# Kernel optimization log

Measured on AMD Instinct MI355X. Metric: run time of the kernel, lower is better.

## Reference

```python
import jax, jax.numpy as jnp
import numpy as np

B, C, H, W = 4, 256, 64, 64
D, K = 256, 32
EPS = 1e-12  # F.normalize clamp

def setup_inputs() -> dict:
    key = jax.random.key(0)
    k1, k2, k3, k4 = jax.random.split(key, 4)
    x = jax.random.normal(k1, (B, C, H, W), dtype=jnp.float32)
    w_theta = jax.random.normal(k2, (D, C), dtype=jnp.float32) * 0.05  # 1x1 conv theta
    w_phi = jax.random.normal(k3, (K, C // K), dtype=jnp.float32) * 0.1  # grouped 1x1 conv phi
    scale = jax.random.uniform(k4, (D, K), dtype=jnp.float32, minval=-1.0, maxval=0.0)
    return {"x": x, "w_theta": w_theta, "w_phi": w_phi, "scale": scale}

def reference(x, w_theta, w_phi, scale):
    b, c, h, w = x.shape
    d, k = scale.shape
    n = h * w
    xf = x.reshape(b, c, n)                                   # B,D,N (C==D)
    # --- Gen_code ---
    xg = xf.reshape(b, k, c // k, n)                          # grouped 1x1 conv
    x_phi = jnp.einsum('bkcn,kc->bnk', xg, w_phi)             # B,N,K
    x_phi = jax.nn.softmax(x_phi, axis=1)                     # softmax over pixels
    x_theta = jnp.einsum('dc,bcn->bdn', w_theta, xf)          # B,D,N
    code = jnp.einsum('bdn,bnk->bdk', x_theta, x_phi)         # B,D,K
    code = code / jnp.maximum(jnp.linalg.norm(code, axis=1, keepdims=True), EPS)
    # (dropout p=0.15 treated as identity)
    # --- embedded residual, without materializing B,N,D,K ---
    s2 = scale * scale                                        # D,K
    t1 = jnp.einsum('bdn,dk->bnk', xf * xf, s2)
    t2 = jnp.einsum('bdn,bdk->bnk', xf, s2[None] * code)
    t3 = jnp.einsum('dk,bdk->bk', s2, code * code)
    dist = t1 - 2.0 * t2 + t3[:, None, :]                     # sum_d (scale*(x-code))^2
    Q = jax.nn.softmax(-0.5 * dist, axis=2)                   # B,N,K
    Qsum = Q.sum(axis=1)                                      # B,K
    # Z_[b,d,k] = sum_n Q*residual / Qsum = scale*(sum_n Q x / Qsum - code)
    Z_ = scale[None] * (jnp.einsum('bdn,bnk->bdk', xf, Q) / Qsum[:, None, :] - code)
    Z = Z_ / jnp.sqrt((Z_ * Z_).sum(axis=1, keepdims=True))   # torch sqrt, no eps
    return Z, Q
```

## Files before the change

kernel.cpp:

```cpp
#include <hip/hip_runtime.h>
#include <math.h>

#define BB 4
#define CC 256
#define NN 4096
#define KK 32
#define DD 256
#define GG 8
#define NT2 64
#define NE 8

__device__ __forceinline__ float wredsum(float v) {
#pragma unroll
  for (int o = 32; o > 0; o >>= 1) v += __shfl_xor(v, o, 64);
  return v;
}

__global__ __launch_bounds__(256) void k_phi(const float* __restrict__ x,
                                             const float* __restrict__ wphi,
                                             float* __restrict__ phi,
                                             float* __restrict__ Sp) {
  const int half = blockIdx.x & 1;
  const int k = (blockIdx.x >> 1) & 31;
  const int b = blockIdx.x >> 6;
  const int tid = threadIdx.x;
  const float* xb = x + (size_t)(b * CC + k * GG) * NN + half * 2048;
  float w[GG];
#pragma unroll
  for (int j = 0; j < GG; ++j) w[j] = wphi[k * GG + j];
  float4 v[2];
  float sum = 0.f;
#pragma unroll
  for (int i = 0; i < 2; ++i) {
    const int n = i * 1024 + tid * 4;
    float4 s = make_float4(0.f, 0.f, 0.f, 0.f);
#pragma unroll
    for (int j = 0; j < GG; ++j) {
      const float4 xv = *reinterpret_cast<const float4*>(xb + (size_t)j * NN + n);
      s.x = fmaf(xv.x, w[j], s.x);
      s.y = fmaf(xv.y, w[j], s.y);
      s.z = fmaf(xv.z, w[j], s.z);
      s.w = fmaf(xv.w, w[j], s.w);
    }
    v[i].x = __expf(s.x);
    v[i].y = __expf(s.y);
    v[i].z = __expf(s.z);
    v[i].w = __expf(s.w);
    sum += v[i].x + v[i].y + v[i].z + v[i].w;
  }
  float* pk = phi + (size_t)(b * KK + k) * NN + half * 2048;
#pragma unroll
  for (int i = 0; i < 2; ++i) {
    *reinterpret_cast<float4*>(pk + i * 1024 + tid * 4) = v[i];
  }
  __shared__ float rb[4];
  sum = wredsum(sum);
  if ((tid & 63) == 0) rb[tid >> 6] = sum;
  __syncthreads();
  if (tid == 0)
    Sp[((size_t)half * BB + b) * KK + k] = rb[0] + rb[1] + rb[2] + rb[3];
}

__global__ __launch_bounds__(256) void k_xpT(const float* __restrict__ x,
                                             const float* __restrict__ phi,
                                             float* __restrict__ m1e) {
  const int e = blockIdx.x & 7;
  const int ct = (blockIdx.x >> 3) & 31;
  const int b = blockIdx.x >> 8;
  const int tid = threadIdx.x;
  __shared__ float smem[256 * 33];
  const int kl = tid >> 3;
  const int nq = tid & 7;
  const int k = tid & 31;
  const int g = tid >> 5;
  const float* xb = x + (size_t)(b * CC + ct * 8) * NN + e * 512;
  float acc[8] = {0.f, 0.f, 0.f, 0.f, 0.f, 0.f, 0.f, 0.f};
#pragma unroll
  for (int ch = 0; ch < 2; ++ch) {
    const float* pch = phi + (size_t)(b * KK + kl) * NN + e * 512 + ch * 256;
#pragma unroll
    for (int j = 0; j < 8; ++j) {
      const int nn = (j * 8 + nq) * 4;
      const float4 pv = *reinterpret_cast<const float4*>(pch + nn);
      smem[(nn + 0) * 33 + kl] = pv.x;
      smem[(nn + 1) * 33 + kl] = pv.y;
      smem[(nn + 2) * 33 + kl] = pv.z;
      smem[(nn + 3) * 33 + kl] = pv.w;
    }
    __syncthreads();
#pragma unroll
    for (int i = 0; i < 8; ++i) {
      const int nl = g * 32 + i * 4;
      const float p0 = smem[(nl + 0) * 33 + k];
      const float p1 = smem[(nl + 1) * 33 + k];
      const float p2 = smem[(nl + 2) * 33 + k];
      const float p3 = smem[(nl + 3) * 33 + k];
#pragma unroll
      for (int c = 0; c < 8; ++c) {
        const float4 xv =
            *reinterpret_cast<const float4*>(xb + (size_t)c * NN + ch * 256 + nl);
        acc[c] = fmaf(xv.x, p0, acc[c]);
        acc[c] = fmaf(xv.y, p1, acc[c]);
        acc[c] = fmaf(xv.z, p2, acc[c]);
        acc[c] = fmaf(xv.w, p3, acc[c]);
      }
    }
    __syncthreads();
  }
#pragma unroll
  for (int c = 0; c < 8; ++c) smem[(g * 8 + c) * 33 + k] = acc[c];
  __syncthreads();
  const int c2 = tid & 7, k2 = tid >> 3;
  float s = 0.f;
#pragma unroll
  for (int gg = 0; gg < 8; ++gg) s += smem[(gg * 8 + c2) * 33 + k2];
  m1e[((size_t)(e * BB + b) * KK + k2) * CC + ct * 8 + c2] = s;
}

__global__ __launch_bounds__(256) void k_code(const float* __restrict__ m1e,
                                              const float* __restrict__ Sp,
                                              const float* __restrict__ wth,
                                              const float* __restrict__ scale,
                                              float* __restrict__ code,
                                              float* __restrict__ bc2,
                                              float* __restrict__ s2g,
                                              float* __restrict__ t3) {
  const int b = blockIdx.x >> 5;
  const int k = blockIdx.x & 31;
  const int d = threadIdx.x;
  const float invS =
      1.f / (Sp[(size_t)b * KK + k] + Sp[((size_t)BB + b) * KK + k]);
  __shared__ __align__(16) float m1s[CC];
  float m = 0.f;
#pragma unroll
  for (int e = 0; e < NE; ++e)
    m += m1e[((size_t)(e * BB + b) * KK + k) * CC + d];
  m1s[d] = m * invS;
  __syncthreads();
  float cd = 0.f;
  const float* wt = wth + (size_t)d * CC;
#pragma unroll 4
  for (int c = 0; c < CC; c += 4) {
    const float4 w4 = *reinterpret_cast<const float4*>(wt + c);
    const float4 m4 = *reinterpret_cast<const float4*>(&m1s[c]);
    cd = fmaf(w4.x, m4.x, cd);
    cd = fmaf(w4.y, m4.y, cd);
    cd = fmaf(w4.z, m4.z, cd);
    cd = fmaf(w4.w, m4.w, cd);
  }
  __shared__ float rb[4];
  float ss = wredsum(cd * cd);
  if ((d & 63) == 0) rb[d >> 6] = ss;
  __syncthreads();
  const float nrm = sqrtf(rb[0] + rb[1] + rb[2] + rb[3]);
  const float inv = 1.f / fmaxf(nrm, 1e-12f);
  cd *= inv;
  const float sc = scale[(size_t)d * KK + k];
  const float s2 = sc * sc;
  code[((size_t)b * DD + d) * KK + k] = cd;
  bc2[((size_t)b * DD + d) * KK + k] = 2.f * s2 * cd;
  if (b == 0) s2g[(size_t)d * KK + k] = s2;
  float tt = wredsum(s2 * cd * cd);
  __syncthreads();
  if ((d & 63) == 0) rb[d >> 6] = tt;
  __syncthreads();
  if (d == 0) t3[b * KK + k] = rb[0] + rb[1] + rb[2] + rb[3];
}

__global__ __launch_bounds__(512) void k_dist(const float* __restrict__ x,
                                              const float* __restrict__ s2g,
                                              const float* __restrict__ bc2,
                                              const float* __restrict__ t3,
                                              float* __restrict__ qout,
                                              float* __restrict__ qpart) {
  const int b = blockIdx.x >> 6;
  const int tile = blockIdx.x & 63;
  const int n0 = tile * 64;
  const int tid = threadIdx.x;
  const int lane = tid & 63;
  const int wid = __builtin_amdgcn_readfirstlane(tid >> 6);
  const int d0 = wid * 32;
  __shared__ float lds[4 * 64 * 33];
  __shared__ float smax[64 * 9];
  __shared__ float ssum[64 * 9];
  float accA[32], accB[32];
#pragma unroll
  for (int k = 0; k < 32; ++k) { accA[k] = 0.f; accB[k] = 0.f; }
  const float* xb = x + ((size_t)b * CC + d0) * NN + n0 + lane;
  const float* s2b = s2g + (size_t)d0 * KK;
  const float* bcb = bc2 + ((size_t)b * DD + d0) * KK;
#pragma unroll 2
  for (int dd = 0; dd < 32; ++dd) {
    const float xv = xb[(size_t)dd * NN];
    const float x2 = xv * xv;
    const float* s2r = s2b + dd * KK;
    const float* bcr = bcb + dd * KK;
#pragma unroll
    for (int k = 0; k < 32; ++k) {
      accA[k] = fmaf(x2, s2r[k], accA[k]);
      accB[k] = fmaf(xv, bcr[k], accB[k]);
    }
  }
  if (wid >= 4) {
    float* Lp = lds + ((size_t)((wid - 4) * 64 + lane)) * 33;
#pragma unroll
    for (int k = 0; k < 32; ++k) Lp[k] = accA[k] - accB[k];
  }
  __syncthreads();
  if (wid < 4) {
    float* Lp = lds + ((size_t)(wid * 64 + lane)) * 33;
#pragma unroll
    for (int k = 0; k < 32; ++k) Lp[k] += accA[k] - accB[k];
  }
  __syncthreads();
  const int n = lane;
  const int kq = wid;
  float vals[4];
#pragma unroll
  for (int j = 0; j < 4; ++j) {
    const int k = kq * 4 + j;
    float s = 0.f;
#pragma unroll
    for (int g = 0; g < 4; ++g) s += lds[((size_t)(g * 64 + n)) * 33 + k];
    vals[j] = -0.5f * (s + t3[b * KK + k]);
  }
  float m4 = fmaxf(fmaxf(vals[0], vals[1]), fmaxf(vals[2], vals[3]));
  smax[n * 9 + kq] = m4;
  __syncthreads();
  float m = smax[n * 9 + 0];
#pragma unroll
  for (int g = 1; g < 8; ++g) m = fmaxf(m, smax[n * 9 + g]);
  float e[4];
  float ps = 0.f;
#pragma unroll
  for (int j = 0; j < 4; ++j) {
    e[j] = __expf(vals[j] - m);
    ps += e[j];
  }
  ssum[n * 9 + kq] = ps;
  __syncthreads();
  float tot = 0.f;
#pragma unroll
  for (int g = 0; g < 8; ++g) tot += ssum[n * 9 + g];
  const float inv = 1.f / tot;
  float4 q4;
  q4.x = e[0] * inv; q4.y = e[1] * inv; q4.z = e[2] * inv; q4.w = e[3] * inv;
  *reinterpret_cast<float4*>(qout + ((size_t)b * NN + n0 + n) * KK + kq * 4) = q4;
  float qs[4] = {q4.x, q4.y, q4.z, q4.w};
#pragma unroll
  for (int j = 0; j < 4; ++j) {
    const float v = wredsum(qs[j]);
    if (n == 0) qpart[((size_t)b * KK + kq * 4 + j) * NT2 + tile] = v;
  }
}

__global__ __launch_bounds__(256) void k_xq(const float* __restrict__ x,
                                            const float* __restrict__ q,
                                            float* __restrict__ znq8) {
  const int e = blockIdx.x & 7;
  const int ct = (blockIdx.x >> 3) & 31;
  const int b = blockIdx.x >> 8;
  const int tid = threadIdx.x;
  const int k = tid & 31;
  const int g = tid >> 5;
  const int n0 = e * 512 + g * 64;
  const float* xb = x + (size_t)(b * CC + ct * 8) * NN;
  const float* qb = q + (size_t)b * NN * KK + k;
  float acc[8] = {0.f, 0.f, 0.f, 0.f, 0.f, 0.f, 0.f, 0.f};
  for (int n = n0; n < n0 + 64; n += 4) {
    const float p0 = qb[(size_t)(n + 0) * KK];
    const float p1 = qb[(size_t)(n + 1) * KK];
    const float p2 = qb[(size_t)(n + 2) * KK];
    const float p3 = qb[(size_t)(n + 3) * KK];
#pragma unroll
    for (int c = 0; c < 8; ++c) {
      const float4 xv = *reinterpret_cast<const float4*>(xb + (size_t)c * NN + n);
      acc[c] = fmaf(xv.x, p0, acc[c]);
      acc[c] = fmaf(xv.y, p1, acc[c]);
      acc[c] = fmaf(xv.z, p2, acc[c]);
      acc[c] = fmaf(xv.w, p3, acc[c]);
    }
  }
  __shared__ float lds[8 * 8 * 33];
#pragma unroll
  for (int c = 0; c < 8; ++c) lds[(g * 8 + c) * 33 + k] = acc[c];
  __syncthreads();
  const int c2 = tid & 7, k2 = tid >> 3;
  float s = 0.f;
#pragma unroll
  for (int gg = 0; gg < 8; ++gg) s += lds[(gg * 8 + c2) * 33 + k2];
  znq8[((size_t)(e * BB + b) * KK + k2) * CC + ct * 8 + c2] = s;
}

__global__ __launch_bounds__(256) void k_z(const float* __restrict__ znq8,
                                           const float* __restrict__ code,
                                           const float* __restrict__ scale,
                                           const float* __restrict__ qpart,
                                           float* __restrict__ zout) {
  const int b = blockIdx.x >> 5;
  const int k = blockIdx.x & 31;
  const int d = threadIdx.x;
  __shared__ float rb[4];
  float qp = 0.f;
  if (d < NT2) qp = qpart[((size_t)b * KK + k) * NT2 + d];
  qp = wredsum(qp);
  if ((d & 63) == 0) rb[d >> 6] = qp;
  __syncthreads();
  const float qs = rb[0] + rb[1] + rb[2] + rb[3];
  float zn = 0.f;
#pragma unroll
  for (int e = 0; e < NE; ++e)
    zn += znq8[((size_t)(e * BB + b) * KK + k) * CC + d];
  const float cd = code[((size_t)b * DD + d) * KK + k];
  const float z_ = scale[(size_t)d * KK + k] * (zn / qs - cd);
  float ss = wredsum(z_ * z_);
  __syncthreads();
  if ((d & 63) == 0) rb[d >> 6] = ss;
  __syncthreads();
  const float rn = 1.f / sqrtf(rb[0] + rb[1] + rb[2] + rb[3]);
  zout[((size_t)b * DD + d) * KK + k] = z_ * rn;
}

extern "C" void kernel_launch(void* const* d_in, const int* in_sizes, int n_in,
                              void* d_out, int out_size, void* d_ws, size_t ws_size,
                              hipStream_t stream) {
  const float* x = (const float*)d_in[0];
  const float* wth = (const float*)d_in[1];
  const float* wphi = (const float*)d_in[2];
  const float* scale = (const float*)d_in[3];
  float* out = (float*)d_out;
  float* zout = out;
  float* qout = out + (size_t)BB * DD * KK;
  float* ws = (float*)d_ws;
  float* phi = ws;
  float* Sp = phi + (size_t)BB * NN * KK;
  float* m1e = Sp + 2 * (size_t)BB * KK;
  float* code = m1e + (size_t)NE * BB * KK * CC;
  float* bc2 = code + (size_t)BB * DD * KK;
  float* s2g = bc2 + (size_t)BB * DD * KK;
  float* t3 = s2g + (size_t)DD * KK;
  float* qpart = t3 + BB * KK;
  float* znq8 = qpart + (size_t)BB * KK * NT2;

  k_phi<<<BB * KK * 2, 256, 0, stream>>>(x, wphi, phi, Sp);
  k_xpT<<<BB * 32 * NE, 256, 0, stream>>>(x, phi, m1e);
  k_code<<<BB * KK, 256, 0, stream>>>(m1e, Sp, wth, scale, code, bc2, s2g, t3);
  k_dist<<<BB * NT2, 512, 0, stream>>>(x, s2g, bc2, t3, qout, qpart);
  k_xq<<<BB * 32 * NE, 256, 0, stream>>>(x, qout, znq8);
  k_z<<<BB * KK, 256, 0, stream>>>(znq8, code, scale, qpart, zout);
}
```

Measured before the change: 78.03 us.

## Fuse epilogue kernels into producers via last-blocks atomic-counter handoff

Merges k_code into k_xpT and k_z into k_xq, cutting the launch count from six to four. Each block increments a global counter after writing its partials. The last 128 blocks to arrive spin until every block has finished, then run the per-(b,k) epilogue. This removes two launches and their gaps, but the handoff costs a spin-wait, and the counters are reset inside k_phi.

```diff
diff --git a/kernel.cpp b/kernel.cpp
--- a/kernel.cpp
+++ b/kernel.cpp
@@ -9,6 +9,8 @@
 #define GG 8
 #define NT2 64
 #define NE 8
+#define XPT_BLOCKS (BB * 32 * NE)
+#define EPI (BB * KK)
 
 __device__ __forceinline__ float wredsum(float v) {
 #pragma unroll
@@ -19,11 +21,16 @@
 __global__ __launch_bounds__(256) void k_phi(const float* __restrict__ x,
                                              const float* __restrict__ wphi,
                                              float* __restrict__ phi,
-                                             float* __restrict__ Sp) {
+                                             float* __restrict__ Sp,
+                                             int* __restrict__ cnts) {
+  const int tid = threadIdx.x;
+  if (blockIdx.x == 0 && tid == 0) {
+    __hip_atomic_store(&cnts[0], 0, __ATOMIC_RELAXED, __HIP_MEMORY_SCOPE_AGENT);
+    __hip_atomic_store(&cnts[1], 0, __ATOMIC_RELAXED, __HIP_MEMORY_SCOPE_AGENT);
+  }
   const int half = blockIdx.x & 1;
   const int k = (blockIdx.x >> 1) & 31;
   const int b = blockIdx.x >> 6;
-  const int tid = threadIdx.x;
   const float* xb = x + (size_t)(b * CC + k * GG) * NN + half * 2048;
   float w[GG];
 #pragma unroll
@@ -61,9 +68,12 @@
     Sp[((size_t)half * BB + b) * KK + k] = rb[0] + rb[1] + rb[2] + rb[3];
 }
 
-__global__ __launch_bounds__(256) void k_xpT(const float* __restrict__ x,
-                                             const float* __restrict__ phi,
-                                             float* __restrict__ m1e) {
+__global__ __launch_bounds__(256) void k_xpT_code(
+    const float* __restrict__ x, const float* __restrict__ phi,
+    float* __restrict__ m1e, const float* __restrict__ Sp,
+    const float* __restrict__ wth, const float* __restrict__ scale,
+    float* __restrict__ code, float* __restrict__ bc2,
+    float* __restrict__ s2g, float* __restrict__ t3, int* __restrict__ cnt) {
   const int e = blockIdx.x & 7;
   const int ct = (blockIdx.x >> 3) & 31;
   const int b = blockIdx.x >> 8;
@@ -110,61 +120,69 @@
 #pragma unroll
   for (int c = 0; c < 8; ++c) smem[(g * 8 + c) * 33 + k] = acc[c];
   __syncthreads();
-  const int c2 = tid & 7, k2 = tid >> 3;
-  float s = 0.f;
-#pragma unroll
-  for (int gg = 0; gg < 8; ++gg) s += smem[(gg * 8 + c2) * 33 + k2];
-  m1e[((size_t)(e * BB + b) * KK + k2) * CC + ct * 8 + c2] = s;
-}
-
-__global__ __launch_bounds__(256) void k_code(const float* __restrict__ m1e,
-                                              const float* __restrict__ Sp,
-                                              const float* __restrict__ wth,
-                                              const float* __restrict__ scale,
-                                              float* __restrict__ code,
-                                              float* __restrict__ bc2,
-                                              float* __restrict__ s2g,
-                                              float* __restrict__ t3) {
-  const int b = blockIdx.x >> 5;
-  const int k = blockIdx.x & 31;
-  const int d = threadIdx.x;
-  const float invS =
-      1.f / (Sp[(size_t)b * KK + k] + Sp[((size_t)BB + b) * KK + k]);
-  __shared__ __align__(16) float m1s[CC];
-  float m = 0.f;
-#pragma unroll
-  for (int e = 0; e < NE; ++e)
-    m += m1e[((size_t)(e * BB + b) * KK + k) * CC + d];
-  m1s[d] = m * invS;
-  __syncthreads();
-  float cd = 0.f;
-  const float* wt = wth + (size_t)d * CC;
+  {
+    const int c2 = tid & 7, k2 = tid >> 3;
+    float s = 0.f;
+#pragma unroll
+    for (int gg = 0; gg < 8; ++gg) s += smem[(gg * 8 + c2) * 33 + k2];
+    m1e[((size_t)(e * BB + b) * KK + k2) * CC + ct * 8 + c2] = s;
+  }
+  __shared__ int srank;
+  __syncthreads();
+  if (tid == 0)
+    srank = __hip_atomic_fetch_add(cnt, 1, __ATOMIC_ACQ_REL,
+                                   __HIP_MEMORY_SCOPE_AGENT);
+  __syncthreads();
+  if (srank < XPT_BLOCKS - EPI) return;
+  const int uid = srank - (XPT_BLOCKS - EPI);
+  const int bb = uid >> 5;
+  const int kk = uid & 31;
+  if (tid == 0) {
+    while (__hip_atomic_load(cnt, __ATOMIC_ACQUIRE,
+                             __HIP_MEMORY_SCOPE_AGENT) < XPT_BLOCKS)
+      __builtin_amdgcn_s_sleep(4);
+  }
+  __syncthreads();
+  (void)__hip_atomic_load(cnt, __ATOMIC_ACQUIRE, __HIP_MEMORY_SCOPE_AGENT);
+  {
+    const int d = tid;
+    float* m1s = smem;
+    __shared__ float rbx[4];
+    const float invS =
+        1.f / (Sp[(size_t)bb * KK + kk] + Sp[((size_t)BB + bb) * KK + kk]);
+    float m = 0.f;
+#pragma unroll
+    for (int e2 = 0; e2 < NE; ++e2)
+      m += m1e[(((size_t)e2 * BB + bb) * KK + kk) * CC + d];
+    m1s[d] = m * invS;
+    __syncthreads();
+    float cd = 0.f;
+    const float* wt = wth + (size_t)d * CC;
 #pragma unroll 4
-  for (int c = 0; c < CC; c += 4) {
-    const float4 w4 = *reinterpret_cast<const float4*>(wt + c);
-    const float4 m4 = *reinterpret_cast<const float4*>(&m1s[c]);
-    cd = fmaf(w4.x, m4.x, cd);
-    cd = fmaf(w4.y, m4.y, cd);
-    cd = fmaf(w4.z, m4.z, cd);
-    cd = fmaf(w4.w, m4.w, cd);
-  }
-  __shared__ float rb[4];
-  float ss = wredsum(cd * cd);
-  if ((d & 63) == 0) rb[d >> 6] = ss;
-  __syncthreads();
-  const float nrm = sqrtf(rb[0] + rb[1] + rb[2] + rb[3]);
-  const float inv = 1.f / fmaxf(nrm, 1e-12f);
-  cd *= inv;
-  const float sc = scale[(size_t)d * KK + k];
-  const float s2 = sc * sc;
-  code[((size_t)b * DD + d) * KK + k] = cd;
-  bc2[((size_t)b * DD + d) * KK + k] = 2.f * s2 * cd;
-  if (b == 0) s2g[(size_t)d * KK + k] = s2;
-  float tt = wredsum(s2 * cd * cd);
-  __syncthreads();
-  if ((d & 63) == 0) rb[d >> 6] = tt;
-  __syncthreads();
-  if (d == 0) t3[b * KK + k] = rb[0] + rb[1] + rb[2] + rb[3];
+    for (int c = 0; c < CC; c += 4) {
+      const float4 w4 = *reinterpret_cast<const float4*>(wt + c);
+      cd = fmaf(w4.x, m1s[c + 0], cd);
+      cd = fmaf(w4.y, m1s[c + 1], cd);
+      cd = fmaf(w4.z, m1s[c + 2], cd);
+      cd = fmaf(w4.w, m1s[c + 3], cd);
+    }
+    float ss = wredsum(cd * cd);
+    if ((d & 63) == 0) rbx[d >> 6] = ss;
+    __syncthreads();
+    const float nrm = sqrtf(rbx[0] + rbx[1] + rbx[2] + rbx[3]);
+    const float inv = 1.f / fmaxf(nrm, 1e-12f);
+    cd *= inv;
+    const float sc = scale[(size_t)d * KK + kk];
+    const float s2 = sc * sc;
+    code[((size_t)bb * DD + d) * KK + kk] = cd;
+    bc2[((size_t)bb * DD + d) * KK + kk] = 2.f * s2 * cd;
+    if (bb == 0) s2g[(size_t)d * KK + kk] = s2;
+    float tt = wredsum(s2 * cd * cd);
+    __syncthreads();
+    if ((d & 63) == 0) rbx[d >> 6] = tt;
+    __syncthreads();
+    if (d == 0) t3[bb * KK + kk] = rbx[0] + rbx[1] + rbx[2] + rbx[3];
+  }
 }
 
 __global__ __launch_bounds__(512) void k_dist(const float* __restrict__ x,
@@ -244,8 +262,10 @@
   for (int g = 0; g < 8; ++g) tot += ssum[n * 9 + g];
   const float inv = 1.f / tot;
   float4 q4;
-  q4.x = e[0] * inv; q4.y = e[1] * inv; q4.z = e[2] * inv; q4.w = e[3] * inv;
-  *reinterpret_cast<float4*>(qout + ((size_t)b * NN + n0 + n) * KK + kq * 4) = q4;
+  q4.x = e[0] * inv; q4.y = e[1] * inv;
+  q4.z = e[2] * inv; q4.w = e[3] * inv;
+  *reinterpret_cast<float4*>(qout + ((size_t)b * NN + n0 + n) * KK + kq * 4) =
+      q4;
   float qs[4] = {q4.x, q4.y, q4.z, q4.w};
 #pragma unroll
   for (int j = 0; j < 4; ++j) {
@@ -254,9 +274,11 @@
   }
 }
 
-__global__ __launch_bounds__(256) void k_xq(const float* __restrict__ x,
-                                            const float* __restrict__ q,
-                                            float* __restrict__ znq8) {
+__global__ __launch_bounds__(256) void k_xq_z(
+    const float* __restrict__ x, const float* __restrict__ q,
+    float* __restrict__ znq8, const float* __restrict__ code,
+    const float* __restrict__ scale, const float* __restrict__ qpart,
+    float* __restrict__ zout, int* __restrict__ cnt) {
   const int e = blockIdx.x & 7;
   const int ct = (blockIdx.x >> 3) & 31;
   const int b = blockIdx.x >> 8;
@@ -285,45 +307,56 @@
 #pragma unroll
   for (int c = 0; c < 8; ++c) lds[(g * 8 + c) * 33 + k] = acc[c];
   __syncthreads();
-  const int c2 = tid & 7, k2 = tid >> 3;
-  float s = 0.f;
-#pragma unroll
-  for (int gg = 0; gg < 8; ++gg) s += lds[(gg * 8 + c2) * 33 + k2];
-  znq8[((size_t)(e * BB + b) * KK + k2) * CC + ct * 8 + c2] = s;
-}
-
-__global__ __launch_bounds__(256) void k_z(const float* __restrict__ znq8,
-                                           const float* __restrict__ code,
-                                           const float* __restrict__ scale,
-                                           const float* __restrict__ qpart,
-                                           float* __restrict__ zout) {
-  const int b = blockIdx.x >> 5;
-  const int k = blockIdx.x & 31;
-  const int d = threadIdx.x;
-  __shared__ float rb[4];
-  float qp = 0.f;
-  if (d < NT2) qp = qpart[((size_t)b * KK + k) * NT2 + d];
-  qp = wredsum(qp);
-  if ((d & 63) == 0) rb[d >> 6] = qp;
-  __syncthreads();
-  const float qs = rb[0] + rb[1] + rb[2] + rb[3];
-  float zn = 0.f;
-#pragma unroll
-  for (int e = 0; e < NE; ++e)
-    zn += znq8[((size_t)(e * BB + b) * KK + k) * CC + d];
-  const float cd = code[((size_t)b * DD + d) * KK + k];
-  const float z_ = scale[(size_t)d * KK + k] * (zn / qs - cd);
-  float ss = wredsum(z_ * z_);
-  __syncthreads();
-  if ((d & 63) == 0) rb[d >> 6] = ss;
-  __syncthreads();
-  const float rn = 1.f / sqrtf(rb[0] + rb[1] + rb[2] + rb[3]);
-  zout[((size_t)b * DD + d) * KK + k] = z_ * rn;
+  {
+    const int c2 = tid & 7, k2 = tid >> 3;
+    float s = 0.f;
+#pragma unroll
+    for (int gg = 0; gg < 8; ++gg) s += lds[(gg * 8 + c2) * 33 + k2];
+    znq8[((size_t)(e * BB + b) * KK + k2) * CC + ct * 8 + c2] = s;
+  }
+  __shared__ int srank;
+  __syncthreads();
+  if (tid == 0)
+    srank = __hip_atomic_fetch_add(cnt, 1, __ATOMIC_ACQ_REL,
+                                   __HIP_MEMORY_SCOPE_AGENT);
+  __syncthreads();
+  if (srank < XPT_BLOCKS - EPI) return;
+  const int uid = srank - (XPT_BLOCKS - EPI);
+  const int bb = uid >> 5;
+  const int kk = uid & 31;
+  if (tid == 0) {
+    while (__hip_atomic_load(cnt, __ATOMIC_ACQUIRE,
+                             __HIP_MEMORY_SCOPE_AGENT) < XPT_BLOCKS)
+      __builtin_amdgcn_s_sleep(4);
+  }
+  __syncthreads();
+  (void)__hip_atomic_load(cnt, __ATOMIC_ACQUIRE, __HIP_MEMORY_SCOPE_AGENT);
+  {
+    const int d = tid;
+    __shared__ float rbx[4];
+    float qp = (d < NT2) ? qpart[((size_t)bb * KK + kk) * NT2 + d] : 0.f;
+    qp = wredsum(qp);
+    if ((d & 63) == 0) rbx[d >> 6] = qp;
+    __syncthreads();
+    const float qs2 = rbx[0] + rbx[1] + rbx[2] + rbx[3];
+    float zn = 0.f;
+#pragma unroll
+    for (int e2 = 0; e2 < NE; ++e2)
+      zn += znq8[(((size_t)e2 * BB + bb) * KK + kk) * CC + d];
+    const float cdv = code[((size_t)bb * DD + d) * KK + kk];
+    const float z_ = scale[(size_t)d * KK + kk] * (zn / qs2 - cdv);
+    float ss = wredsum(z_ * z_);
+    __syncthreads();
+    if ((d & 63) == 0) rbx[d >> 6] = ss;
+    __syncthreads();
+    const float rn = 1.f / sqrtf(rbx[0] + rbx[1] + rbx[2] + rbx[3]);
+    zout[((size_t)bb * DD + d) * KK + kk] = z_ * rn;
+  }
 }
 
 extern "C" void kernel_launch(void* const* d_in, const int* in_sizes, int n_in,
-                              void* d_out, int out_size, void* d_ws, size_t ws_size,
-                              hipStream_t stream) {
+                              void* d_out, int out_size, void* d_ws,
+                              size_t ws_size, hipStream_t stream) {
   const float* x = (const float*)d_in[0];
   const float* wth = (const float*)d_in[1];
   const float* wphi = (const float*)d_in[2];
@@ -341,11 +374,12 @@
   float* t3 = s2g + (size_t)DD * KK;
   float* qpart = t3 + BB * KK;
   float* znq8 = qpart + (size_t)BB * KK * NT2;
-
-  k_phi<<<BB * KK * 2, 256, 0, stream>>>(x, wphi, phi, Sp);
-  k_xpT<<<BB * 32 * NE, 256, 0, stream>>>(x, phi, m1e);
-  k_code<<<BB * KK, 256, 0, stream>>>(m1e, Sp, wth, scale, code, bc2, s2g, t3);
+  int* cnts = (int*)(znq8 + (size_t)NE * BB * KK * CC);
+
+  k_phi<<<BB * KK * 2, 256, 0, stream>>>(x, wphi, phi, Sp, cnts);
+  k_xpT_code<<<XPT_BLOCKS, 256, 0, stream>>>(x, phi, m1e, Sp, wth, scale, code,
+                                             bc2, s2g, t3, cnts);
   k_dist<<<BB * NT2, 512, 0, stream>>>(x, s2g, bc2, t3, qout, qpart);
-  k_xq<<<BB * 32 * NE, 256, 0, stream>>>(x, qout, znq8);
-  k_z<<<BB * KK, 256, 0, stream>>>(znq8, code, scale, qpart, zout);
-}
+  k_xq_z<<<XPT_BLOCKS, 256, 0, stream>>>(x, qout, znq8, code, scale, qpart,
+                                         zout, cnts + 1);
+}
```

Result: slower. 146.1 us (+87.3%).

## Store phi pixel-major and reuse one x-times-weights kernel for phi and Q

Applied to the files above, without the earlier changes.

k_phi now tiles over 64-pixel slices and computes all 32 groups per block. It transposes the exp values through LDS so phi is stored in the same [B,N,K] layout as Q, and it writes one partial sum per slice that k_code reduces. This lets the old k_xpT, with its LDS transpose and barriers, be replaced by the same simple k_xp kernel already used for x·Q. k_code also splits its dot-product accumulator into four chains for more instruction-level parallelism. The trade-off is strided 32-float loads of phi in k_xp instead of an LDS-staged transpose, and more partial sums to reduce.

```diff
diff --git a/kernel.cpp b/kernel.cpp
--- a/kernel.cpp
+++ b/kernel.cpp
@@ -9,6 +9,7 @@
 #define GG 8
 #define NT2 64
 #define NE 8
+#define NSL 64
 
 __device__ __forceinline__ float wredsum(float v) {
 #pragma unroll
@@ -19,106 +20,115 @@
 __global__ __launch_bounds__(256) void k_phi(const float* __restrict__ x,
                                              const float* __restrict__ wphi,
                                              float* __restrict__ phi,
-                                             float* __restrict__ Sp) {
-  const int half = blockIdx.x & 1;
-  const int k = (blockIdx.x >> 1) & 31;
+                                             float* __restrict__ SpE) {
   const int b = blockIdx.x >> 6;
+  const int sl = blockIdx.x & 63;
+  const int n0 = sl * 64;
   const int tid = threadIdx.x;
-  const float* xb = x + (size_t)(b * CC + k * GG) * NN + half * 2048;
-  float w[GG];
-#pragma unroll
-  for (int j = 0; j < GG; ++j) w[j] = wphi[k * GG + j];
-  float4 v[2];
-  float sum = 0.f;
-#pragma unroll
-  for (int i = 0; i < 2; ++i) {
-    const int n = i * 1024 + tid * 4;
-    float4 s = make_float4(0.f, 0.f, 0.f, 0.f);
+  __shared__ float phis[64 * 33];
+  __shared__ float sred[8 * 33];
+  {
+    const int kk = tid >> 3;
+    const int m = tid & 7;
+    const float* xb = x + (size_t)(b * CC + kk * GG) * NN + n0 + m * 8;
+    float w[GG];
+#pragma unroll
+    for (int j = 0; j < GG; ++j) w[j] = wphi[kk * GG + j];
+    float4 s0 = make_float4(0.f, 0.f, 0.f, 0.f);
+    float4 s1 = make_float4(0.f, 0.f, 0.f, 0.f);
 #pragma unroll
     for (int j = 0; j < GG; ++j) {
-      const float4 xv = *reinterpret_cast<const float4*>(xb + (size_t)j * NN + n);
-      s.x = fmaf(xv.x, w[j], s.x);
-      s.y = fmaf(xv.y, w[j], s.y);
-      s.z = fmaf(xv.z, w[j], s.z);
-      s.w = fmaf(xv.w, w[j], s.w);
+      const float4 xa = *reinterpret_cast<const float4*>(xb + (size_t)j * NN);
+      const float4 xc = *reinterpret_cast<const float4*>(xb + (size_t)j * NN + 4);
+      s0.x = fmaf(xa.x, w[j], s0.x);
+      s0.y = fmaf(xa.y, w[j], s0.y);
+      s0.z = fmaf(xa.z, w[j], s0.z);
+      s0.w = fmaf(xa.w, w[j], s0.w);
+      s1.x = fmaf(xc.x, w[j], s1.x);
+      s1.y = fmaf(xc.y, w[j], s1.y);
+      s1.z = fmaf(xc.z, w[j], s1.z);
+      s1.w = fmaf(xc.w, w[j], s1.w);
     }
-    v[i].x = __expf(s.x);
-    v[i].y = __expf(s.y);
-    v[i].z = __expf(s.z);
-    v[i].w = __expf(s.w);
-    sum += v[i].x + v[i].y + v[i].z + v[i].w;
-  }
-  float* pk = phi + (size_t)(b * KK + k) * NN + half * 2048;
-#pragma unroll
-  for (int i = 0; i < 2; ++i) {
-    *reinterpret_cast<float4*>(pk + i * 1024 + tid * 4) = v[i];
-  }
-  __shared__ float rb[4];
-  sum = wredsum(sum);
-  if ((tid & 63) == 0) rb[tid >> 6] = sum;
-  __syncthreads();
-  if (tid == 0)
-    Sp[((size_t)half * BB + b) * KK + k] = rb[0] + rb[1] + rb[2] + rb[3];
-}
-
-__global__ __launch_bounds__(256) void k_xpT(const float* __restrict__ x,
-                                             const float* __restrict__ phi,
-                                             float* __restrict__ m1e) {
+    const int nb = m * 8;
+    phis[(nb + 0) * 33 + kk] = __expf(s0.x);
+    phis[(nb + 1) * 33 + kk] = __expf(s0.y);
+    phis[(nb + 2) * 33 + kk] = __expf(s0.z);
+    phis[(nb + 3) * 33 + kk] = __expf(s0.w);
+    phis[(nb + 4) * 33 + kk] = __expf(s1.x);
+    phis[(nb + 5) * 33 + kk] = __expf(s1.y);
+    phis[(nb + 6) * 33 + kk] = __expf(s1.z);
+    phis[(nb + 7) * 33 + kk] = __expf(s1.w);
+  }
+  __syncthreads();
+  {
+    const int k = tid & 31;
+    const int g = tid >> 5;
+    float s = 0.f;
+#pragma unroll
+    for (int i = 0; i < 8; ++i) s += phis[(g * 8 + i) * 33 + k];
+    sred[g * 33 + k] = s;
+  }
+  __syncthreads();
+  {
+    const int n = tid >> 2;
+    const int k0 = (tid & 3) * 8;
+    float v[8];
+#pragma unroll
+    for (int j = 0; j < 8; ++j) v[j] = phis[n * 33 + k0 + j];
+    float* dst = phi + ((size_t)b * NN + n0 + n) * KK + k0;
+    float4 o0 = make_float4(v[0], v[1], v[2], v[3]);
+    float4 o1 = make_float4(v[4], v[5], v[6], v[7]);
+    *reinterpret_cast<float4*>(dst + 0) = o0;
+    *reinterpret_cast<float4*>(dst + 4) = o1;
+    if (tid < 32) {
+      float s = 0.f;
+#pragma unroll
+      for (int g = 0; g < 8; ++g) s += sred[g * 33 + tid];
+      SpE[((size_t)sl * BB + b) * KK + tid] = s;
+    }
+  }
+}
+
+__global__ __launch_bounds__(256) void k_xp(const float* __restrict__ x,
+                                            const float* __restrict__ p,
+                                            float* __restrict__ outq) {
   const int e = blockIdx.x & 7;
   const int ct = (blockIdx.x >> 3) & 31;
   const int b = blockIdx.x >> 8;
   const int tid = threadIdx.x;
-  __shared__ float smem[256 * 33];
-  const int kl = tid >> 3;
-  const int nq = tid & 7;
   const int k = tid & 31;
   const int g = tid >> 5;
-  const float* xb = x + (size_t)(b * CC + ct * 8) * NN + e * 512;
+  const int n0 = e * 512 + g * 64;
+  const float* xb = x + (size_t)(b * CC + ct * 8) * NN;
+  const float* pb = p + (size_t)b * NN * KK + k;
   float acc[8] = {0.f, 0.f, 0.f, 0.f, 0.f, 0.f, 0.f, 0.f};
-#pragma unroll
-  for (int ch = 0; ch < 2; ++ch) {
-    const float* pch = phi + (size_t)(b * KK + kl) * NN + e * 512 + ch * 256;
-#pragma unroll
-    for (int j = 0; j < 8; ++j) {
-      const int nn = (j * 8 + nq) * 4;
-      const float4 pv = *reinterpret_cast<const float4*>(pch + nn);
-      smem[(nn + 0) * 33 + kl] = pv.x;
-      smem[(nn + 1) * 33 + kl] = pv.y;
-      smem[(nn + 2) * 33 + kl] = pv.z;
-      smem[(nn + 3) * 33 + kl] = pv.w;
+  for (int n = n0; n < n0 + 64; n += 4) {
+    const float p0 = pb[(size_t)(n + 0) * KK];
+    const float p1 = pb[(size_t)(n + 1) * KK];
+    const float p2 = pb[(size_t)(n + 2) * KK];
+    const float p3 = pb[(size_t)(n + 3) * KK];
+#pragma unroll
+    for (int c = 0; c < 8; ++c) {
+      const float4 xv = *reinterpret_cast<const float4*>(xb + (size_t)c * NN + n);
+      acc[c] = fmaf(xv.x, p0, acc[c]);
+      acc[c] = fmaf(xv.y, p1, acc[c]);
+      acc[c] = fmaf(xv.z, p2, acc[c]);
+      acc[c] = fmaf(xv.w, p3, acc[c]);
     }
-    __syncthreads();
-#pragma unroll
-    for (int i = 0; i < 8; ++i) {
-      const int nl = g * 32 + i * 4;
-      const float p0 = smem[(nl + 0) * 33 + k];
-      const float p1 = smem[(nl + 1) * 33 + k];
-      const float p2 = smem[(nl + 2) * 33 + k];
-      const float p3 = smem[(nl + 3) * 33 + k];
-#pragma unroll
-      for (int c = 0; c < 8; ++c) {
-        const float4 xv =
-            *reinterpret_cast<const float4*>(xb + (size_t)c * NN + ch * 256 + nl);
-        acc[c] = fmaf(xv.x, p0, acc[c]);
-        acc[c] = fmaf(xv.y, p1, acc[c]);
-        acc[c] = fmaf(xv.z, p2, acc[c]);
-        acc[c] = fmaf(xv.w, p3, acc[c]);
-      }
-    }
-    __syncthreads();
-  }
-#pragma unroll
-  for (int c = 0; c < 8; ++c) smem[(g * 8 + c) * 33 + k] = acc[c];
+  }
+  __shared__ float lds[8 * 8 * 33];
+#pragma unroll
+  for (int c = 0; c < 8; ++c) lds[(g * 8 + c) * 33 + k] = acc[c];
   __syncthreads();
   const int c2 = tid & 7, k2 = tid >> 3;
   float s = 0.f;
 #pragma unroll
-  for (int gg = 0; gg < 8; ++gg) s += smem[(gg * 8 + c2) * 33 + k2];
-  m1e[((size_t)(e * BB + b) * KK + k2) * CC + ct * 8 + c2] = s;
+  for (int gg = 0; gg < 8; ++gg) s += lds[(gg * 8 + c2) * 33 + k2];
+  outq[((size_t)(e * BB + b) * KK + k2) * CC + ct * 8 + c2] = s;
 }
 
 __global__ __launch_bounds__(256) void k_code(const float* __restrict__ m1e,
-                                              const float* __restrict__ Sp,
+                                              const float* __restrict__ SpE,
                                               const float* __restrict__ wth,
                                               const float* __restrict__ scale,
                                               float* __restrict__ code,
@@ -128,28 +138,33 @@
   const int b = blockIdx.x >> 5;
   const int k = blockIdx.x & 31;
   const int d = threadIdx.x;
-  const float invS =
-      1.f / (Sp[(size_t)b * KK + k] + Sp[((size_t)BB + b) * KK + k]);
   __shared__ __align__(16) float m1s[CC];
+  __shared__ float rb[4];
+  float sp = (d < NSL) ? SpE[((size_t)d * BB + b) * KK + k] : 0.f;
+  sp = wredsum(sp);
+  if ((d & 63) == 0) rb[d >> 6] = sp;
+  __syncthreads();
+  const float invS = 1.f / (rb[0] + rb[1] + rb[2] + rb[3]);
   float m = 0.f;
 #pragma unroll
   for (int e = 0; e < NE; ++e)
     m += m1e[((size_t)(e * BB + b) * KK + k) * CC + d];
   m1s[d] = m * invS;
   __syncthreads();
-  float cd = 0.f;
+  float c0 = 0.f, c1 = 0.f, c2 = 0.f, c3 = 0.f;
   const float* wt = wth + (size_t)d * CC;
 #pragma unroll 4
   for (int c = 0; c < CC; c += 4) {
     const float4 w4 = *reinterpret_cast<const float4*>(wt + c);
     const float4 m4 = *reinterpret_cast<const float4*>(&m1s[c]);
-    cd = fmaf(w4.x, m4.x, cd);
-    cd = fmaf(w4.y, m4.y, cd);
-    cd = fmaf(w4.z, m4.z, cd);
-    cd = fmaf(w4.w, m4.w, cd);
-  }
-  __shared__ float rb[4];
+    c0 = fmaf(w4.x, m4.x, c0);
+    c1 = fmaf(w4.y, m4.y, c1);
+    c2 = fmaf(w4.z, m4.z, c2);
+    c3 = fmaf(w4.w, m4.w, c3);
+  }
+  float cd = (c0 + c1) + (c2 + c3);
   float ss = wredsum(cd * cd);
+  __syncthreads();
   if ((d & 63) == 0) rb[d >> 6] = ss;
   __syncthreads();
   const float nrm = sqrtf(rb[0] + rb[1] + rb[2] + rb[3]);
@@ -244,52 +259,16 @@
   for (int g = 0; g < 8; ++g) tot += ssum[n * 9 + g];
   const float inv = 1.f / tot;
   float4 q4;
-  q4.x = e[0] * inv; q4.y = e[1] * inv; q4.z = e[2] * inv; q4.w = e[3] * inv;
-  *reinterpret_cast<float4*>(qout + ((size_t)b * NN + n0 + n) * KK + kq * 4) = q4;
+  q4.x = e[0] * inv; q4.y = e[1] * inv;
+  q4.z = e[2] * inv; q4.w = e[3] * inv;
+  *reinterpret_cast<float4*>(qout + ((size_t)b * NN + n0 + n) * KK + kq * 4) =
+      q4;
   float qs[4] = {q4.x, q4.y, q4.z, q4.w};
 #pragma unroll
   for (int j = 0; j < 4; ++j) {
     const float v = wredsum(qs[j]);
     if (n == 0) qpart[((size_t)b * KK + kq * 4 + j) * NT2 + tile] = v;
   }
-}
-
-__global__ __launch_bounds__(256) void k_xq(const float* __restrict__ x,
-                                            const float* __restrict__ q,
-                                            float* __restrict__ znq8) {
-  const int e = blockIdx.x & 7;
-  const int ct = (blockIdx.x >> 3) & 31;
-  const int b = blockIdx.x >> 8;
-  const int tid = threadIdx.x;
-  const int k = tid & 31;
-  const int g = tid >> 5;
-  const int n0 = e * 512 + g * 64;
-  const float* xb = x + (size_t)(b * CC + ct * 8) * NN;
-  const float* qb = q + (size_t)b * NN * KK + k;
-  float acc[8] = {0.f, 0.f, 0.f, 0.f, 0.f, 0.f, 0.f, 0.f};
-  for (int n = n0; n < n0 + 64; n += 4) {
-    const float p0 = qb[(size_t)(n + 0) * KK];
-    const float p1 = qb[(size_t)(n + 1) * KK];
-    const float p2 = qb[(size_t)(n + 2) * KK];
-    const float p3 = qb[(size_t)(n + 3) * KK];
-#pragma unroll
-    for (int c = 0; c < 8; ++c) {
-      const float4 xv = *reinterpret_cast<const float4*>(xb + (size_t)c * NN + n);
-      acc[c] = fmaf(xv.x, p0, acc[c]);
-      acc[c] = fmaf(xv.y, p1, acc[c]);
-      acc[c] = fmaf(xv.z, p2, acc[c]);
-      acc[c] = fmaf(xv.w, p3, acc[c]);
-    }
-  }
-  __shared__ float lds[8 * 8 * 33];
-#pragma unroll
-  for (int c = 0; c < 8; ++c) lds[(g * 8 + c) * 33 + k] = acc[c];
-  __syncthreads();
-  const int c2 = tid & 7, k2 = tid >> 3;
-  float s = 0.f;
-#pragma unroll
-  for (int gg = 0; gg < 8; ++gg) s += lds[(gg * 8 + c2) * 33 + k2];
-  znq8[((size_t)(e * BB + b) * KK + k2) * CC + ct * 8 + c2] = s;
 }
 
 __global__ __launch_bounds__(256) void k_z(const float* __restrict__ znq8,
@@ -301,8 +280,7 @@
   const int k = blockIdx.x & 31;
   const int d = threadIdx.x;
   __shared__ float rb[4];
-  float qp = 0.f;
-  if (d < NT2) qp = qpart[((size_t)b * KK + k) * NT2 + d];
+  float qp = (d < NT2) ? qpart[((size_t)b * KK + k) * NT2 + d] : 0.f;
   qp = wredsum(qp);
   if ((d & 63) == 0) rb[d >> 6] = qp;
   __syncthreads();
@@ -322,8 +300,8 @@
 }
 
 extern "C" void kernel_launch(void* const* d_in, const int* in_sizes, int n_in,
-                              void* d_out, int out_size, void* d_ws, size_t ws_size,
-                              hipStream_t stream) {
+                              void* d_out, int out_size, void* d_ws,
+                              size_t ws_size, hipStream_t stream) {
   const float* x = (const float*)d_in[0];
   const float* wth = (const float*)d_in[1];
   const float* wphi = (const float*)d_in[2];
@@ -333,8 +311,8 @@
   float* qout = out + (size_t)BB * DD * KK;
   float* ws = (float*)d_ws;
   float* phi = ws;
-  float* Sp = phi + (size_t)BB * NN * KK;
-  float* m1e = Sp + 2 * (size_t)BB * KK;
+  float* SpE = phi + (size_t)BB * NN * KK;
+  float* m1e = SpE + (size_t)NSL * BB * KK;
   float* code = m1e + (size_t)NE * BB * KK * CC;
   float* bc2 = code + (size_t)BB * DD * KK;
   float* s2g = bc2 + (size_t)BB * DD * KK;
@@ -342,10 +320,10 @@
   float* qpart = t3 + BB * KK;
   float* znq8 = qpart + (size_t)BB * KK * NT2;
 
-  k_phi<<<BB * KK * 2, 256, 0, stream>>>(x, wphi, phi, Sp);
-  k_xpT<<<BB * 32 * NE, 256, 0, stream>>>(x, phi, m1e);
-  k_code<<<BB * KK, 256, 0, stream>>>(m1e, Sp, wth, scale, code, bc2, s2g, t3);
+  k_phi<<<BB * NSL, 256, 0, stream>>>(x, wphi, phi, SpE);
+  k_xp<<<BB * 32 * NE, 256, 0, stream>>>(x, phi, m1e);
+  k_code<<<BB * KK, 256, 0, stream>>>(m1e, SpE, wth, scale, code, bc2, s2g, t3);
   k_dist<<<BB * NT2, 512, 0, stream>>>(x, s2g, bc2, t3, qout, qpart);
-  k_xq<<<BB * 32 * NE, 256, 0, stream>>>(x, qout, znq8);
+  k_xp<<<BB * 32 * NE, 256, 0, stream>>>(x, qout, znq8);
   k_z<<<BB * KK, 256, 0, stream>>>(znq8, code, scale, qpart, zout);
 }
```

After: 78.18 us. No clear change (+0.2%).
